# Kernel optimization log

Measured on AMD Instinct MI355X. Metric: run time of the kernel, lower is better.

Reference implementation:

```python
import jax, jax.numpy as jnp
import numpy as np

C, H, W = 3, 2048, 2048
N_BOXES = 256
HEIGHT = 32  # target_height


def _make_boxes():
    # Realistic text-line quads: TL, TR, BR, BL corners.
    rng = np.random.RandomState(0)
    x0 = rng.uniform(0, W - 500, N_BOXES)
    y0 = rng.uniform(0, H - 60, N_BOXES)
    bw = rng.uniform(100, 400, N_BOXES)
    bh = rng.uniform(20, 40, N_BOXES)
    p0 = np.stack([x0, y0], -1)
    p1 = np.stack([x0 + bw, y0], -1)
    p2 = np.stack([x0 + bw, y0 + bh], -1)
    p3 = np.stack([x0, y0 + bh], -1)
    return np.stack([p0, p1, p2, p3], 1).astype(np.float32)  # [N,4,2]


def setup_inputs() -> dict:
    key = jax.random.key(0)
    img = jax.random.normal(key, (C, H, W), dtype=jnp.float32)
    boxes = jnp.asarray(_make_boxes())
    scale = jnp.ones((1,), dtype=jnp.float32)
    return {"img": img, "boxes": boxes, "scale": scale}


def reference(img, boxes, scale):
    height = HEIGHT
    boxes = boxes / scale  # [N,4,2]
    img_c, img_h, img_w = img.shape

    h_dists = jnp.linalg.norm(boxes[:, 2] - boxes[:, 1], axis=1)
    w_dists = jnp.linalg.norm(boxes[:, 1] - boxes[:, 0], axis=1)
    # torch .long() truncates toward zero; values are positive here.
    widths = (height * w_dists / jnp.clip(h_dists, 1e-6)).astype(jnp.int32)
    max_w = int(widths.max()) // 8 * 8 + 8  # concrete (data-dependent shape)

    rows = jnp.arange(height, dtype=jnp.float32) / (height - 1)
    cols = jnp.arange(max_w, dtype=jnp.float32)
    y = rows[None, :, None]        # broadcasts to [N,height,max_w]
    x_idx = cols[None, None, :]
    curr_w = widths.astype(jnp.float32)[:, None, None]
    x = x_idx / jnp.clip(curr_w - 1.0, 1.0)

    def _interp(idx):
        v0 = boxes[:, 0, idx][:, None, None]
        v1 = boxes[:, 1, idx][:, None, None]
        v2 = boxes[:, 2, idx][:, None, None]
        v3 = boxes[:, 3, idx][:, None, None]
        return (1 - x) * (1 - y) * v0 + x * (1 - y) * v1 + x * y * v2 + (1 - x) * y * v3

    res_x = _interp(0)  # [N,height,max_w]
    res_y = _interp(1)
    mask = x_idx < curr_w
    grid_c = jnp.where(mask, res_x / (img_w - 1.0) * 2.0 - 1.0, 2.0)
    grid_r = jnp.where(mask, res_y / (img_h - 1.0) * 2.0 - 1.0, 2.0)

    # grid_sample(mode='nearest', padding_mode='zeros', align_corners=True)
    ix = jnp.round((grid_c + 1.0) * (img_w - 1) * 0.5)
    iy = jnp.round((grid_r + 1.0) * (img_h - 1) * 0.5)
    inb = (ix >= 0) & (ix <= img_w - 1) & (iy >= 0) & (iy <= img_h - 1)
    ixc = jnp.clip(ix, 0, img_w - 1).astype(jnp.int32)
    iyc = jnp.clip(iy, 0, img_h - 1).astype(jnp.int32)
    samp = img[:, iyc, ixc]                    # [C,N,height,max_w]
    out = jnp.where(inb[None], samp, 0.0).transpose(1, 0, 2, 3)  # [N,C,height,max_w]

    widths_out = (widths // 8 * 8 + 8).astype(jnp.int32)
    return out, widths_out
```

## Files before the change

### kernel.cpp

```cpp
#include <hip/hip_runtime.h>

constexpr int kC = 3;
constexpr int kH = 2048;
constexpr int kW = 2048;
constexpr int kNB = 256;
constexpr int kHeight = 32;

typedef float f32x4 __attribute__((ext_vector_type(4)));

__global__ __launch_bounds__(64) void extract_kernel(
    const float* __restrict__ img,
    const float* __restrict__ boxes,
    const float* __restrict__ scale,
    float* __restrict__ out,
    int max_w)
{
#pragma clang fp contract(off)
    const int r = blockIdx.y;
    const int b = blockIdx.z;
    const int c0 = (blockIdx.x * 64 + threadIdx.x) * 4;
    if (c0 >= max_w) return;

    const float s = scale[0];
    const float* bx = boxes + b * 8;
    const float p0x = bx[0] / s, p0y = bx[1] / s;
    const float p1x = bx[2] / s, p1y = bx[3] / s;
    const float p2x = bx[4] / s, p2y = bx[5] / s;
    const float p3x = bx[6] / s, p3y = bx[7] / s;

    const float hdx = p2x - p1x, hdy = p2y - p1y;
    const float h_dist = sqrtf(hdx * hdx + hdy * hdy);
    const float wdx = p1x - p0x, wdy = p1y - p0y;
    const float w_dist = sqrtf(wdx * wdx + wdy * wdy);
    const int width = (int)(32.0f * w_dist / fmaxf(h_dist, 1e-6f));
    const float curr_w = (float)width;

    if (r == 0 && c0 == 0) {
        out[(size_t)kNB * kC * kHeight * max_w + b] = (float)(width / 8 * 8 + 8);
    }

    const size_t ch_stride = (size_t)kHeight * max_w;
    const size_t obase = (((size_t)b * kC) * (size_t)kHeight + (size_t)r) * (size_t)max_w + (size_t)c0;

    f32x4 o0 = {0.f, 0.f, 0.f, 0.f};
    f32x4 o1 = {0.f, 0.f, 0.f, 0.f};
    f32x4 o2 = {0.f, 0.f, 0.f, 0.f};

    if (c0 < width) {
        const float y = (float)r / 31.0f;
        const float omy = 1.0f - y;
        const float xden = fmaxf(curr_w - 1.0f, 1.0f);
#pragma unroll
        for (int j = 0; j < 4; ++j) {
            const float cf = (float)(c0 + j);
            if (cf < curr_w) {
                const float x = cf / xden;
                const float omx = 1.0f - x;
                const float w00 = omx * omy;
                const float w10 = x * omy;
                const float w11 = x * y;
                const float w01 = omx * y;
                const float res_x = w00 * p0x + w10 * p1x + w11 * p2x + w01 * p3x;
                const float res_y = w00 * p0y + w10 * p1y + w11 * p2y + w01 * p3y;

                const float grid_c = res_x / 2047.0f * 2.0f - 1.0f;
                const float grid_r = res_y / 2047.0f * 2.0f - 1.0f;
                const float fix = rintf((grid_c + 1.0f) * 2047.0f * 0.5f);
                const float fiy = rintf((grid_r + 1.0f) * 2047.0f * 0.5f);
                const bool inb = (fix >= 0.0f) && (fix <= 2047.0f) &&
                                 (fiy >= 0.0f) && (fiy <= 2047.0f);
                const int ixc = (int)fminf(fmaxf(fix, 0.0f), 2047.0f);
                const int iyc = (int)fminf(fmaxf(fiy, 0.0f), 2047.0f);

                const size_t ipix = (size_t)iyc * kW + (size_t)ixc;
                const float v0 = img[ipix];
                const float v1 = img[(size_t)kH * kW + ipix];
                const float v2 = img[2 * (size_t)kH * kW + ipix];
                o0[j] = inb ? v0 : 0.0f;
                o1[j] = inb ? v1 : 0.0f;
                o2[j] = inb ? v2 : 0.0f;
            }
        }
    }

    __builtin_nontemporal_store(o0, (f32x4*)(out + obase));
    __builtin_nontemporal_store(o1, (f32x4*)(out + obase + ch_stride));
    __builtin_nontemporal_store(o2, (f32x4*)(out + obase + 2 * ch_stride));
}

extern "C" void kernel_launch(void* const* d_in, const int* in_sizes, int n_in,
                              void* d_out, int out_size, void* d_ws, size_t ws_size,
                              hipStream_t stream) {
    const float* img   = (const float*)d_in[0];
    const float* boxes = (const float*)d_in[1];
    const float* scale = (const float*)d_in[2];
    float* out = (float*)d_out;

    const int max_w = (out_size - kNB) / (kNB * kC * kHeight);
    const int quads = max_w / 4;

    dim3 grid((quads + 63) / 64, kHeight, kNB);
    extract_kernel<<<grid, dim3(64, 1, 1), 0, stream>>>(img, boxes, scale, out, max_w);
}
```

Baseline: 23.76 us.

## Split padding zero-fill into dedicated blocks and gather only valid columns

The kernel is now launched on a flat 1D grid with two roles. Dedicated fill blocks, one per (box, channel, 8-row group), write zeros to the padded region beyond each box's width. Gather blocks exit early when their columns lie beyond the box width, so blocks covering mostly padding skip the per-pixel coordinate math. This moves padding writes out of the gather path at the cost of a second code path, plain rather than nontemporal stores for the fill, and per-block index decoding.

New measurement: 24.78 us. +4.3%, slower.

```diff
diff --git a/kernel.cpp b/kernel.cpp
--- a/kernel.cpp
+++ b/kernel.cpp
@@ -8,36 +8,77 @@
 
 typedef float f32x4 __attribute__((ext_vector_type(4)));
 
-__global__ __launch_bounds__(64) void extract_kernel(
+struct BoxParams {
+    float p0x, p0y, p1x, p1y, p2x, p2y, p3x, p3y;
+    float curr_w;
+    int width;
+};
+
+__device__ __forceinline__ BoxParams box_params(const float* __restrict__ boxes,
+                                                const float* __restrict__ scale,
+                                                int b) {
+#pragma clang fp contract(off)
+    const float s = scale[0];
+    const float* bx = boxes + b * 8;
+    BoxParams P;
+    P.p0x = bx[0] / s; P.p0y = bx[1] / s;
+    P.p1x = bx[2] / s; P.p1y = bx[3] / s;
+    P.p2x = bx[4] / s; P.p2y = bx[5] / s;
+    P.p3x = bx[6] / s; P.p3y = bx[7] / s;
+    const float hdx = P.p2x - P.p1x, hdy = P.p2y - P.p1y;
+    const float h_dist = sqrtf(hdx * hdx + hdy * hdy);
+    const float wdx = P.p1x - P.p0x, wdy = P.p1y - P.p0y;
+    const float w_dist = sqrtf(wdx * wdx + wdy * wdy);
+    P.width = (int)(32.0f * w_dist / fmaxf(h_dist, 1e-6f));
+    P.curr_w = (float)P.width;
+    return P;
+}
+
+__global__ __launch_bounds__(64) void extract_fused_kernel(
     const float* __restrict__ img,
     const float* __restrict__ boxes,
     const float* __restrict__ scale,
     float* __restrict__ out,
-    int max_w)
+    int max_w, int nq, int nqc, int fillBlocks)
 {
 #pragma clang fp contract(off)
-    const int r = blockIdx.y;
-    const int b = blockIdx.z;
-    const int c0 = (blockIdx.x * 64 + threadIdx.x) * 4;
-    if (c0 >= max_w) return;
+    const int bid = blockIdx.x;
 
-    const float s = scale[0];
-    const float* bx = boxes + b * 8;
-    const float p0x = bx[0] / s, p0y = bx[1] / s;
-    const float p1x = bx[2] / s, p1y = bx[3] / s;
-    const float p2x = bx[4] / s, p2y = bx[5] / s;
-    const float p3x = bx[6] / s, p3y = bx[7] / s;
+    if (bid < fillBlocks) {
+        const int rg = bid & 3;
+        const int chb = bid >> 2;
+        const int b = chb / 3;
+        const int ch = chb - b * 3;
 
-    const float hdx = p2x - p1x, hdy = p2y - p1y;
-    const float h_dist = sqrtf(hdx * hdx + hdy * hdy);
-    const float wdx = p1x - p0x, wdy = p1y - p0y;
-    const float w_dist = sqrtf(wdx * wdx + wdy * wdy);
-    const int width = (int)(32.0f * w_dist / fmaxf(h_dist, 1e-6f));
-    const float curr_w = (float)width;
+        const BoxParams P = box_params(boxes, scale, b);
+        const int qstart = (P.width + 3) >> 2;
 
-    if (r == 0 && c0 == 0) {
-        out[(size_t)kNB * kC * kHeight * max_w + b] = (float)(width / 8 * 8 + 8);
+        if (ch == 0 && rg == 0 && threadIdx.x == 0) {
+            out[(size_t)kNB * kC * kHeight * max_w + b] =
+                (float)(P.width / 8 * 8 + 8);
+        }
+
+        float* plane = out + (size_t)(b * kC + ch) * kHeight * max_w;
+        const f32x4 z = {0.f, 0.f, 0.f, 0.f};
+#pragma unroll
+        for (int rr = 0; rr < 8; ++rr) {
+            float* rowp = plane + (size_t)(rg * 8 + rr) * max_w;
+            for (int q = qstart + threadIdx.x; q < nq; q += 64) {
+                *(f32x4*)(rowp + q * 4) = z;
+            }
+        }
+        return;
     }
+
+    const int gid = bid - fillBlocks;
+    const int qc = gid % nqc;
+    const int rb = gid / nqc;
+    const int r = rb & 31;
+    const int b = rb >> 5;
+
+    const BoxParams P = box_params(boxes, scale, b);
+    const int c0 = (qc * 64 + threadIdx.x) * 4;
+    if (c0 >= P.width) return;
 
     const size_t ch_stride = (size_t)kHeight * max_w;
     const size_t obase = (((size_t)b * kC) * (size_t)kHeight + (size_t)r) * (size_t)max_w + (size_t)c0;
@@ -46,40 +87,38 @@
     f32x4 o1 = {0.f, 0.f, 0.f, 0.f};
     f32x4 o2 = {0.f, 0.f, 0.f, 0.f};
 
-    if (c0 < width) {
-        const float y = (float)r / 31.0f;
-        const float omy = 1.0f - y;
-        const float xden = fmaxf(curr_w - 1.0f, 1.0f);
+    const float y = (float)r / 31.0f;
+    const float omy = 1.0f - y;
+    const float xden = fmaxf(P.curr_w - 1.0f, 1.0f);
 #pragma unroll
-        for (int j = 0; j < 4; ++j) {
-            const float cf = (float)(c0 + j);
-            if (cf < curr_w) {
-                const float x = cf / xden;
-                const float omx = 1.0f - x;
-                const float w00 = omx * omy;
-                const float w10 = x * omy;
-                const float w11 = x * y;
-                const float w01 = omx * y;
-                const float res_x = w00 * p0x + w10 * p1x + w11 * p2x + w01 * p3x;
-                const float res_y = w00 * p0y + w10 * p1y + w11 * p2y + w01 * p3y;
+    for (int j = 0; j < 4; ++j) {
+        const float cf = (float)(c0 + j);
+        if (cf < P.curr_w) {
+            const float x = cf / xden;
+            const float omx = 1.0f - x;
+            const float w00 = omx * omy;
+            const float w10 = x * omy;
+            const float w11 = x * y;
+            const float w01 = omx * y;
+            const float res_x = w00 * P.p0x + w10 * P.p1x + w11 * P.p2x + w01 * P.p3x;
+            const float res_y = w00 * P.p0y + w10 * P.p1y + w11 * P.p2y + w01 * P.p3y;
 
-                const float grid_c = res_x / 2047.0f * 2.0f - 1.0f;
-                const float grid_r = res_y / 2047.0f * 2.0f - 1.0f;
-                const float fix = rintf((grid_c + 1.0f) * 2047.0f * 0.5f);
-                const float fiy = rintf((grid_r + 1.0f) * 2047.0f * 0.5f);
-                const bool inb = (fix >= 0.0f) && (fix <= 2047.0f) &&
-                                 (fiy >= 0.0f) && (fiy <= 2047.0f);
-                const int ixc = (int)fminf(fmaxf(fix, 0.0f), 2047.0f);
-                const int iyc = (int)fminf(fmaxf(fiy, 0.0f), 2047.0f);
+            const float grid_c = res_x / 2047.0f * 2.0f - 1.0f;
+            const float grid_r = res_y / 2047.0f * 2.0f - 1.0f;
+            const float fix = rintf((grid_c + 1.0f) * 2047.0f * 0.5f);
+            const float fiy = rintf((grid_r + 1.0f) * 2047.0f * 0.5f);
+            const bool inb = (fix >= 0.0f) && (fix <= 2047.0f) &&
+                             (fiy >= 0.0f) && (fiy <= 2047.0f);
+            const int ixc = (int)fminf(fmaxf(fix, 0.0f), 2047.0f);
+            const int iyc = (int)fminf(fmaxf(fiy, 0.0f), 2047.0f);
 
-                const size_t ipix = (size_t)iyc * kW + (size_t)ixc;
-                const float v0 = img[ipix];
-                const float v1 = img[(size_t)kH * kW + ipix];
-                const float v2 = img[2 * (size_t)kH * kW + ipix];
-                o0[j] = inb ? v0 : 0.0f;
-                o1[j] = inb ? v1 : 0.0f;
-                o2[j] = inb ? v2 : 0.0f;
-            }
+            const size_t ipix = (size_t)iyc * kW + (size_t)ixc;
+            const float v0 = img[ipix];
+            const float v1 = img[(size_t)kH * kW + ipix];
+            const float v2 = img[2 * (size_t)kH * kW + ipix];
+            o0[j] = inb ? v0 : 0.0f;
+            o1[j] = inb ? v1 : 0.0f;
+            o2[j] = inb ? v2 : 0.0f;
         }
     }
 
@@ -97,8 +136,13 @@
     float* out = (float*)d_out;
 
     const int max_w = (out_size - kNB) / (kNB * kC * kHeight);
-    const int quads = max_w / 4;
+    const int nq = max_w / 4;
+    const int nqc = (nq + 63) / 64;
 
-    dim3 grid((quads + 63) / 64, kHeight, kNB);
-    extract_kernel<<<grid, dim3(64, 1, 1), 0, stream>>>(img, boxes, scale, out, max_w);
+    const int fillBlocks = kNB * kC * 4;
+    const int gatherBlocks = nqc * kHeight * kNB;
+    const int nblocks = fillBlocks + gatherBlocks;
+
+    extract_fused_kernel<<<nblocks, 64, 0, stream>>>(img, boxes, scale, out,
+                                                     max_w, nq, nqc, fillBlocks);
 }
```
